# Kernel tuning notes

Hardware: AMD Instinct MI355X
Metric: run time of the kernel (lower is better)

## Reference

```python
import jax, jax.numpy as jnp
import numpy as np

B, T, H, D = 512, 256, 256, 3  # batch, seq_len, RNN_hid_dim, var_dim


def setup_inputs() -> dict:
    key = jax.random.key(0)
    ks = jax.random.split(key, 14)
    s = 1.0 / np.sqrt(H)  # PyTorch GRU init scale
    return {
        "X_p": jax.random.normal(ks[0], (B, T, D), jnp.float32),
        "X_f": jax.random.normal(ks[1], (B, T, D), jnp.float32),
        "noise": jax.random.normal(ks[2], (1, B, H), jnp.float32),
        # encoder GRU params (PyTorch layout: gates ordered r, z, n)
        "W_ih_enc": jax.random.uniform(ks[3], (3 * H, D), jnp.float32, -s, s),
        "W_hh_enc": jax.random.uniform(ks[4], (3 * H, H), jnp.float32, -s, s),
        "b_ih_enc": jax.random.uniform(ks[5], (3 * H,), jnp.float32, -s, s),
        "b_hh_enc": jax.random.uniform(ks[6], (3 * H,), jnp.float32, -s, s),
        # decoder GRU params
        "W_ih_dec": jax.random.uniform(ks[7], (3 * H, D), jnp.float32, -s, s),
        "W_hh_dec": jax.random.uniform(ks[8], (3 * H, H), jnp.float32, -s, s),
        "b_ih_dec": jax.random.uniform(ks[9], (3 * H,), jnp.float32, -s, s),
        "b_hh_dec": jax.random.uniform(ks[10], (3 * H,), jnp.float32, -s, s),
        # output projection
        "W_fc": jax.random.uniform(ks[11], (D, H), jnp.float32, -s, s),
        "b_fc": jax.random.uniform(ks[12], (D,), jnp.float32, -s, s),
    }


def _gru(x, h0, W_ih, W_hh, b_ih, b_hh):
    # x: [B, T, D]; h0: [B, H]. PyTorch GRU cell math, gate order r, z, n.
    xg = jnp.einsum('btd,gd->btg', x, W_ih) + b_ih  # [B, T, 3H] (one big GEMM)

    def step(h, xg_t):
        gh = h @ W_hh.T + b_hh                      # [B, 3H]
        xr, xz, xn = jnp.split(xg_t, 3, axis=-1)
        hr, hz, hn = jnp.split(gh, 3, axis=-1)
        r = jax.nn.sigmoid(xr + hr)
        z = jax.nn.sigmoid(xz + hz)
        n = jnp.tanh(xn + r * hn)
        h_new = (1.0 - z) * n + z * h
        return h_new, h_new

    hT, ys = jax.lax.scan(step, h0, jnp.swapaxes(xg, 0, 1))  # scan over T
    return jnp.swapaxes(ys, 0, 1), hT  # [B, T, H], [B, H]


def reference(X_p, X_f, noise, W_ih_enc, W_hh_enc, b_ih_enc, b_hh_enc,
              W_ih_dec, W_hh_dec, b_ih_dec, b_hh_dec, W_fc, b_fc):
    h0 = jnp.zeros((X_p.shape[0], W_hh_enc.shape[1]), X_p.dtype)
    _, h_t = _gru(X_p, h0, W_ih_enc, W_hh_enc, b_ih_enc, b_hh_enc)
    hidden = h_t + noise[0]                                   # h_t: [B,H], noise: [1,B,H]
    # shift right by one timestep, zero-fill first step
    X_f_shft = jnp.concatenate(
        [jnp.zeros_like(X_f[:, :1, :]), X_f[:, :-1, :]], axis=1)
    Y_f, _ = _gru(X_f_shft, hidden, W_ih_dec, W_hh_dec, b_ih_dec, b_hh_dec)
    return jnp.einsum('bth,dh->btd', Y_f, W_fc) + b_fc        # [B, T, D]
```

## Files before the change

### kernel.cpp

```cpp
#include <hip/hip_runtime.h>


#define B_TOT 512
#define T_LEN 256
#define HID 256
#define NBATCH 16
#define NB 4
#define NTHREADS 1024
#define NBLK (B_TOT / NB)

#define WR_OFF 0
#define H_OFF  32768
#define X_OFF  40960
#define RD_OFF 57408
#define SMEM_SHORTS (RD_OFF + 16 * 512)
#define SMEM_BYTES  (SMEM_SHORTS * 2)

#define XT 64
#define XSLOTS (T_LEN + 1)
#define HBUF (NBATCH * HID)

typedef __attribute__((ext_vector_type(4))) float f32x4;
typedef __attribute__((ext_vector_type(8))) short shortx8;
typedef __attribute__((ext_vector_type(4))) short i16x4;
typedef __attribute__((ext_vector_type(4))) unsigned short ushortx4;
typedef __attribute__((ext_vector_type(8))) unsigned short ushortx8;

#if __has_builtin(__builtin_amdgcn_mfma_f32_16x16x16_bf16)
#define HAVE_K16 1
#define MFMA_X(A, B, C) __builtin_amdgcn_mfma_f32_16x16x16_bf16((A), (B), (C), 0, 0, 0)
#elif __has_builtin(__builtin_amdgcn_mfma_f32_16x16x16bf16_1k)
#define HAVE_K16 1
#define MFMA_X(A, B, C) __builtin_amdgcn_mfma_f32_16x16x16bf16_1k((A), (B), (C), 0, 0, 0)
#else
#define HAVE_K16 0
#endif

__device__ __forceinline__ unsigned short f2bf(float x) {
    unsigned u = __float_as_uint(x);
    u += 0x7FFF + ((u >> 16) & 1);
    return (unsigned short)(u >> 16);
}
__device__ __forceinline__ float bf2f(unsigned short s) {
    return __uint_as_float(((unsigned)s) << 16);
}
__device__ __forceinline__ float fastrcp(float x) {
#if __has_builtin(__builtin_amdgcn_rcpf)
    return __builtin_amdgcn_rcpf(x);
#else
    return 1.0f / x;
#endif
}
__device__ __forceinline__ float exp2raw(float y) {
#if __has_builtin(__builtin_amdgcn_exp2f)
    return __builtin_amdgcn_exp2f(y);
#else
    return __expf(y * 0.69314718056f);
#endif
}
__device__ __forceinline__ float sigmoid_(float x) {
    return fastrcp(1.0f + exp2raw(x * -1.44269504f));
}
__device__ __forceinline__ float tanh_(float x) {
    return 2.0f * fastrcp(1.0f + exp2raw(x * -2.88539008f)) - 1.0f;
}

__global__ __launch_bounds__(256) void prep_wr(
    const float* __restrict__ Whh_enc, const float* __restrict__ Whh_dec,
    unsigned short* __restrict__ wr_enc, unsigned short* __restrict__ wr_dec)
{
    int idx = blockIdx.x * 256 + threadIdx.x;
    int gru = idx >> 12;
    int rem = idx & 4095;
    int lane = rem & 63;
    int kk = (rem >> 6) & 3;
    int ht = rem >> 8;
    const float* W = gru ? Whh_dec : Whh_enc;
    unsigned short* dst = gru ? wr_dec : wr_enc;
    int row = ht * 16 + (lane & 15);
    int col = (kk + 4) * 32 + (lane >> 4) * 8;
    const float* src = W + (size_t)row * 256 + col;
    ushortx8 v;
    #pragma unroll
    for (int j = 0; j < 8; ++j) v[j] = f2bf(src[j]);
    *(ushortx8*)(dst + (size_t)rem * 8) = v;
}

template<int IS_DEC>
__global__ __launch_bounds__(NTHREADS, 4) void gru_persistent(
    const float* __restrict__ X,
    const float* __restrict__ W_hh,
    const float* __restrict__ W_ih,
    const float* __restrict__ b_ih,
    const float* __restrict__ b_hh,
    const unsigned short* __restrict__ Wr4,
    const float* __restrict__ h_in,
    const float* __restrict__ noise,
    float* __restrict__ h_out,
    unsigned short* __restrict__ Yout)
{
    extern __shared__ unsigned short smem[];
    unsigned short* shWr = smem + WR_OFF;
    unsigned short* shH  = smem + H_OFF;
    unsigned short* shX  = smem + X_OFF;
    unsigned short* shRd = smem + RD_OFF;

    const int tid  = threadIdx.x;
    const int g    = blockIdx.x;
    const int w    = tid >> 6;
    const int lane = tid & 63;
    const int c    = lane & 15;
    const int q    = lane >> 4;
    const int ht   = w;
    const int cv   = lane >> 4;
    const int din  = lane & 15;
    const int d_glob = ht * 16 + din;

    for (int idx = tid; idx < NBATCH * XSLOTS; idx += NTHREADS) {
        int t = idx >> 4, cc = idx & 15;
        int ts = IS_DEC ? (t - 1) : t;
        float x0 = 0.0f, x1 = 0.0f, x2 = 0.0f;
        if (cc < NB && ts >= 0 && ts < T_LEN) {
            const float* xp = X + ((size_t)(g * NB + cc) * T_LEN + ts) * 3;
            x0 = xp[0]; x1 = xp[1]; x2 = xp[2];
        }
        ushortx4 v = {f2bf(x0), f2bf(x1), f2bf(x2), (unsigned short)0x3F80};
        *(ushortx4*)&shX[t * XT + cc * 4] = v;
    }

    {
        int row = ht * 16 + c;
        const float* wp = W_hh + (size_t)row * 256 + q * 8;
        #pragma unroll
        for (int k = 0; k < 4; ++k) {
            const f32x4* p = (const f32x4*)(wp + k * 32);
            f32x4 f0 = p[0];
            f32x4 f1 = p[1];
            shortx8 a;
            a[0] = (short)f2bf(f0[0]); a[1] = (short)f2bf(f0[1]);
            a[2] = (short)f2bf(f0[2]); a[3] = (short)f2bf(f0[3]);
            a[4] = (short)f2bf(f1[0]); a[5] = (short)f2bf(f1[1]);
            a[6] = (short)f2bf(f1[2]); a[7] = (short)f2bf(f1[3]);
            *(shortx8*)&shWr[((ht * 4 + k) * 64 + lane) * 8] = a;
        }
    }

    shortx8 Wf[2][8];
    #pragma unroll
    for (int gg = 0; gg < 2; ++gg) {
        int row = (gg + 1) * 256 + ht * 16 + c;
        const float* wp = W_hh + (size_t)row * 256 + q * 8;
        #pragma unroll
        for (int k = 0; k < 8; ++k) {
            const f32x4* p = (const f32x4*)(wp + k * 32);
            f32x4 f0 = p[0];
            f32x4 f1 = p[1];
            shortx8 a;
            a[0] = (short)f2bf(f0[0]); a[1] = (short)f2bf(f0[1]);
            a[2] = (short)f2bf(f0[2]); a[3] = (short)f2bf(f0[3]);
            a[4] = (short)f2bf(f1[0]); a[5] = (short)f2bf(f1[1]);
            a[6] = (short)f2bf(f1[2]); a[7] = (short)f2bf(f1[3]);
            Wf[gg][k] = a;
        }
    }

#if HAVE_K16
    i16x4 ax[3];
#else
    shortx8 ax[3];
#endif
    {
        int rr_ = ht * 16 + c;
        int rowr = rr_, rowz = 256 + rr_, rown = 512 + rr_;
        short r0 = 0, r1 = 0, r2 = 0, r3 = 0, z0 = 0, z1 = 0, z2 = 0, z3 = 0;
        short n0 = 0, n1 = 0, n2 = 0, n3 = 0;
        if (q == 0) {
            r0 = (short)f2bf(W_ih[rowr * 3 + 0]);
            r1 = (short)f2bf(W_ih[rowr * 3 + 1]);
            r2 = (short)f2bf(W_ih[rowr * 3 + 2]);
            r3 = (short)f2bf(b_ih[rowr] + b_hh[rowr]);
            z0 = (short)f2bf(W_ih[rowz * 3 + 0]);
            z1 = (short)f2bf(W_ih[rowz * 3 + 1]);
            z2 = (short)f2bf(W_ih[rowz * 3 + 2]);
            z3 = (short)f2bf(b_ih[rowz] + b_hh[rowz]);
            n0 = (short)f2bf(W_ih[rown * 3 + 0]);
            n1 = (short)f2bf(W_ih[rown * 3 + 1]);
            n2 = (short)f2bf(W_ih[rown * 3 + 2]);
            n3 = (short)f2bf(b_ih[rown]);
        }
#if HAVE_K16
        ax[0] = i16x4{r0, r1, r2, r3};
        ax[1] = i16x4{z0, z1, z2, z3};
        ax[2] = i16x4{n0, n1, n2, n3};
#else
        ax[0] = shortx8{r0, r1, r2, r3, 0, 0, 0, 0};
        ax[1] = shortx8{z0, z1, z2, z3, 0, 0, 0, 0};
        ax[2] = shortx8{n0, n1, n2, n3, 0, 0, 0, 0};
#endif
    }

    f32x4 nhb = *(const f32x4*)(b_hh + 512 + ht * 16 + q * 4);

    const int offv = ht * 256 + (din >> 3) * 128 + ((din >> 2) & 1) * 4
                   + cv * 8 + (din & 3);

    {
        const ushortx8 z8 = {0, 0, 0, 0, 0, 0, 0, 0};
        *(ushortx8*)&shH[tid * 8] = z8;
    }
    __syncthreads();

    float hold = 0.0f;
    if (IS_DEC) {
        int b = g * NB + cv;
        hold = h_in[(size_t)b * HID + d_glob] + noise[(size_t)b * HID + d_glob];
        shH[offv] = f2bf(hold);
    }

    unsigned short* yp = nullptr;
    if (IS_DEC)
        yp = Yout + ((size_t)g * T_LEN * NB + cv) * HID + d_glob;

    __syncthreads();

    const f32x4 zc = {0.0f, 0.0f, 0.0f, 0.0f};

    f32x4 acc0, acc1, acc2, acc3;
    {
#if HAVE_K16
        i16x4 bx = *(const i16x4*)&shX[c * 4];
        acc0 = MFMA_X(ax[0], bx, zc);
        acc1 = MFMA_X(ax[1], bx, zc);
        acc3 = MFMA_X(ax[2], bx, zc);
#else
        ushortx4 xv = *(const ushortx4*)&shX[c * 4];
        shortx8 bx = (q == 0)
            ? shortx8{(short)xv[0], (short)xv[1], (short)xv[2], (short)xv[3], 0, 0, 0, 0}
            : shortx8{0, 0, 0, 0, 0, 0, 0, 0};
        acc0 = __builtin_amdgcn_mfma_f32_16x16x32_bf16(ax[0], bx, zc, 0, 0, 0);
        acc1 = __builtin_amdgcn_mfma_f32_16x16x32_bf16(ax[1], bx, zc, 0, 0, 0);
        acc3 = __builtin_amdgcn_mfma_f32_16x16x32_bf16(ax[2], bx, zc, 0, 0, 0);
#endif
    }

    const int bbase = q * 128 + c * 8;
    const unsigned short* ab = shWr + ((size_t)(ht * 4) * 64 + lane) * 8;
    const unsigned short* gb = Wr4 + ((size_t)(ht * 4) * 64 + lane) * 8;
    unsigned short* shRd_w = shRd + w * 512;

    int xidx = XT + c * 4;

    for (int t = 0; t < T_LEN; ++t) {
        const unsigned short* brow = shH + (t & 1) * HBUF + bbase;
        unsigned short* hn = shH + ((t + 1) & 1) * HBUF;

        shortx8 gr[4];
        #pragma unroll
        for (int kk = 0; kk < 4; ++kk)
            gr[kk] = *(const shortx8*)(gb + kk * 512);

        acc2 = nhb;

        #pragma unroll
        for (int k = 0; k < 4; ++k) {
            shortx8 bf = *(const shortx8*)(brow + k * 512);
            shortx8 ar = *(const shortx8*)(ab + k * 512);
            acc0 = __builtin_amdgcn_mfma_f32_16x16x32_bf16(ar,       bf, acc0, 0, 0, 0);
            acc1 = __builtin_amdgcn_mfma_f32_16x16x32_bf16(Wf[0][k], bf, acc1, 0, 0, 0);
            acc2 = __builtin_amdgcn_mfma_f32_16x16x32_bf16(Wf[1][k], bf, acc2, 0, 0, 0);
        }
        #pragma unroll
        for (int k = 4; k < 8; ++k) {
            shortx8 bf = *(const shortx8*)(brow + k * 512);
            acc0 = __builtin_amdgcn_mfma_f32_16x16x32_bf16(gr[k - 4], bf, acc0, 0, 0, 0);
            acc1 = __builtin_amdgcn_mfma_f32_16x16x32_bf16(Wf[0][k],  bf, acc1, 0, 0, 0);
            acc2 = __builtin_amdgcn_mfma_f32_16x16x32_bf16(Wf[1][k],  bf, acc2, 0, 0, 0);
        }

        if (c < NB) {
            #pragma unroll
            for (int r = 0; r < 4; ++r) {
                f32x4 v = {acc0[r], acc1[r], acc2[r], acc3[r]};
                *(f32x4*)&shRd_w[(c * 16 + q * 4 + r) * 8] = v;
            }
        }

#if HAVE_K16
        i16x4 bxn = *(const i16x4*)&shX[xidx];
#else
        ushortx4 xvn = *(const ushortx4*)&shX[xidx];
        shortx8 bxn = (q == 0)
            ? shortx8{(short)xvn[0], (short)xvn[1], (short)xvn[2], (short)xvn[3], 0, 0, 0, 0}
            : shortx8{0, 0, 0, 0, 0, 0, 0, 0};
#endif
        xidx += XT;

#if HAVE_K16
        acc0 = MFMA_X(ax[0], bxn, zc);
        acc1 = MFMA_X(ax[1], bxn, zc);
        acc3 = MFMA_X(ax[2], bxn, zc);
#else
        acc0 = __builtin_amdgcn_mfma_f32_16x16x32_bf16(ax[0], bxn, zc, 0, 0, 0);
        acc1 = __builtin_amdgcn_mfma_f32_16x16x32_bf16(ax[1], bxn, zc, 0, 0, 0);
        acc3 = __builtin_amdgcn_mfma_f32_16x16x32_bf16(ax[2], bxn, zc, 0, 0, 0);
#endif

        {
            f32x4 av = *(const f32x4*)&shRd_w[lane * 8];
            float rr = sigmoid_(av[0]);
            float zz = sigmoid_(av[1]);
            float nn = tanh_(av[3] + rr * av[2]);
            float ho = nn + zz * (hold - nn);
            hold = ho;
            unsigned short hb = f2bf(ho);
            hn[offv] = hb;
            if (IS_DEC) {
                *yp = hb;
                yp += NB * HID;
            }
        }
        __syncthreads();
    }

    if (!IS_DEC) {
        h_out[(size_t)(g * NB + cv) * HID + d_glob] = hold;
    }
}

__global__ __launch_bounds__(256) void proj_kernel(
    const unsigned short* __restrict__ Y, const float* __restrict__ W_fc,
    const float* __restrict__ b_fc, float* __restrict__ out)
{
    int row = blockIdx.x * 256 + threadIdx.x;
    int b4 = row & (NB - 1);
    int gt = row >> 2;
    int t = gt & (T_LEN - 1);
    int g = gt >> 8;
    const unsigned short* y = Y + (size_t)row * HID;
    float a0 = b_fc[0], a1 = b_fc[1], a2 = b_fc[2];
    #pragma unroll 4
    for (int k8 = 0; k8 < 32; ++k8) {
        ushortx8 v = *(const ushortx8*)(y + k8 * 8);
        #pragma unroll
        for (int j = 0; j < 8; ++j) {
            float f = bf2f(v[j]);
            int k = k8 * 8 + j;
            a0 += f * W_fc[k];
            a1 += f * W_fc[256 + k];
            a2 += f * W_fc[512 + k];
        }
    }
    int batch = g * NB + b4;
    float* o = out + ((size_t)batch * T_LEN + t) * 3;
    o[0] = a0; o[1] = a1; o[2] = a2;
}

extern "C" void kernel_launch(void* const* d_in, const int* in_sizes, int n_in,
                              void* d_out, int out_size, void* d_ws, size_t ws_size,
                              hipStream_t stream)
{
    const float* X_p      = (const float*)d_in[0];
    const float* X_f      = (const float*)d_in[1];
    const float* noise    = (const float*)d_in[2];
    const float* W_ih_enc = (const float*)d_in[3];
    const float* W_hh_enc = (const float*)d_in[4];
    const float* b_ih_enc = (const float*)d_in[5];
    const float* b_hh_enc = (const float*)d_in[6];
    const float* W_ih_dec = (const float*)d_in[7];
    const float* W_hh_dec = (const float*)d_in[8];
    const float* b_ih_dec = (const float*)d_in[9];
    const float* b_hh_dec = (const float*)d_in[10];
    const float* W_fc     = (const float*)d_in[11];
    const float* b_fc     = (const float*)d_in[12];

    (void)hipFuncSetAttribute((const void*)&gru_persistent<0>,
                              hipFuncAttributeMaxDynamicSharedMemorySize, SMEM_BYTES);
    (void)hipFuncSetAttribute((const void*)&gru_persistent<1>,
                              hipFuncAttributeMaxDynamicSharedMemorySize, SMEM_BYTES);

    float* h_enc = (float*)d_ws;
    unsigned short* wr_enc = (unsigned short*)((char*)d_ws + (512u << 10));
    unsigned short* wr_dec = (unsigned short*)((char*)d_ws + (576u << 10));
    unsigned short* Yws    = (unsigned short*)((char*)d_ws + (640u << 10));

    hipLaunchKernelGGL(prep_wr, dim3(32), dim3(256), 0, stream,
        W_hh_enc, W_hh_dec, wr_enc, wr_dec);

    hipLaunchKernelGGL((gru_persistent<0>), dim3(NBLK), dim3(NTHREADS), SMEM_BYTES, stream,
        X_p, W_hh_enc, W_ih_enc, b_ih_enc, b_hh_enc, wr_enc,
        (const float*)nullptr, (const float*)nullptr, h_enc,
        (unsigned short*)nullptr);

    hipLaunchKernelGGL((gru_persistent<1>), dim3(NBLK), dim3(NTHREADS), SMEM_BYTES, stream,
        X_f, W_hh_dec, W_ih_dec, b_ih_dec, b_hh_dec, wr_dec,
        h_enc, noise, (float*)nullptr, Yws);

    hipLaunchKernelGGL(proj_kernel, dim3((B_TOT * T_LEN) / 256), dim3(256), 0, stream,
        Yws, W_fc, b_fc, (float*)d_out);
}
```

Measured before the change: 943.7 us.

## Keep all recurrent weights in registers and shrink LDS to the real batch

Moves the r-gate slice of W_hh, previously split between LDS and a global prep buffer, into registers, so each wave keeps all three gates' weight fragments resident. This drops the prep_wr kernel and the per-step global and LDS weight reads. The hidden-state and input buffers are sized for the 4 real batch columns instead of 16, so LDS use falls and the dynamic shared-memory attribute call is removed. It also adds an XOR swizzle on the gate-exchange scratch to avoid bank conflicts. The cost is higher register pressure from 24 resident weight fragments per thread, which may cause spills at 1024 threads.

```diff
diff --git a/kernel.cpp b/kernel.cpp
--- a/kernel.cpp
+++ b/kernel.cpp
@@ -9,16 +9,15 @@
 #define NTHREADS 1024
 #define NBLK (B_TOT / NB)
 
-#define WR_OFF 0
-#define H_OFF  32768
-#define X_OFF  40960
-#define RD_OFF 57408
+#define XSLOTS (T_LEN + 1)
+#define XT 16
+#define HBUF (NB * HID)
+
+#define H_OFF 0
+#define X_OFF (2 * HBUF)
+#define RD_OFF (X_OFF + XSLOTS * XT)
 #define SMEM_SHORTS (RD_OFF + 16 * 512)
 #define SMEM_BYTES  (SMEM_SHORTS * 2)
-
-#define XT 64
-#define XSLOTS (T_LEN + 1)
-#define HBUF (NBATCH * HID)
 
 typedef __attribute__((ext_vector_type(4))) float f32x4;
 typedef __attribute__((ext_vector_type(8))) short shortx8;
@@ -63,27 +62,6 @@
 }
 __device__ __forceinline__ float tanh_(float x) {
     return 2.0f * fastrcp(1.0f + exp2raw(x * -2.88539008f)) - 1.0f;
-}
-
-__global__ __launch_bounds__(256) void prep_wr(
-    const float* __restrict__ Whh_enc, const float* __restrict__ Whh_dec,
-    unsigned short* __restrict__ wr_enc, unsigned short* __restrict__ wr_dec)
-{
-    int idx = blockIdx.x * 256 + threadIdx.x;
-    int gru = idx >> 12;
-    int rem = idx & 4095;
-    int lane = rem & 63;
-    int kk = (rem >> 6) & 3;
-    int ht = rem >> 8;
-    const float* W = gru ? Whh_dec : Whh_enc;
-    unsigned short* dst = gru ? wr_dec : wr_enc;
-    int row = ht * 16 + (lane & 15);
-    int col = (kk + 4) * 32 + (lane >> 4) * 8;
-    const float* src = W + (size_t)row * 256 + col;
-    ushortx8 v;
-    #pragma unroll
-    for (int j = 0; j < 8; ++j) v[j] = f2bf(src[j]);
-    *(ushortx8*)(dst + (size_t)rem * 8) = v;
 }
 
 template<int IS_DEC>
@@ -93,14 +71,12 @@
     const float* __restrict__ W_ih,
     const float* __restrict__ b_ih,
     const float* __restrict__ b_hh,
-    const unsigned short* __restrict__ Wr4,
     const float* __restrict__ h_in,
     const float* __restrict__ noise,
     float* __restrict__ h_out,
     unsigned short* __restrict__ Yout)
 {
     extern __shared__ unsigned short smem[];
-    unsigned short* shWr = smem + WR_OFF;
     unsigned short* shH  = smem + H_OFF;
     unsigned short* shX  = smem + X_OFF;
     unsigned short* shRd = smem + RD_OFF;
@@ -116,11 +92,11 @@
     const int din  = lane & 15;
     const int d_glob = ht * 16 + din;
 
-    for (int idx = tid; idx < NBATCH * XSLOTS; idx += NTHREADS) {
-        int t = idx >> 4, cc = idx & 15;
+    for (int idx = tid; idx < NB * XSLOTS; idx += NTHREADS) {
+        int t = idx >> 2, cc = idx & 3;
         int ts = IS_DEC ? (t - 1) : t;
         float x0 = 0.0f, x1 = 0.0f, x2 = 0.0f;
-        if (cc < NB && ts >= 0 && ts < T_LEN) {
+        if (ts >= 0 && ts < T_LEN) {
             const float* xp = X + ((size_t)(g * NB + cc) * T_LEN + ts) * 3;
             x0 = xp[0]; x1 = xp[1]; x2 = xp[2];
         }
@@ -128,27 +104,10 @@
         *(ushortx4*)&shX[t * XT + cc * 4] = v;
     }
 
-    {
-        int row = ht * 16 + c;
-        const float* wp = W_hh + (size_t)row * 256 + q * 8;
-        #pragma unroll
-        for (int k = 0; k < 4; ++k) {
-            const f32x4* p = (const f32x4*)(wp + k * 32);
-            f32x4 f0 = p[0];
-            f32x4 f1 = p[1];
-            shortx8 a;
-            a[0] = (short)f2bf(f0[0]); a[1] = (short)f2bf(f0[1]);
-            a[2] = (short)f2bf(f0[2]); a[3] = (short)f2bf(f0[3]);
-            a[4] = (short)f2bf(f1[0]); a[5] = (short)f2bf(f1[1]);
-            a[6] = (short)f2bf(f1[2]); a[7] = (short)f2bf(f1[3]);
-            *(shortx8*)&shWr[((ht * 4 + k) * 64 + lane) * 8] = a;
-        }
-    }
-
-    shortx8 Wf[2][8];
+    shortx8 Wf[3][8];
     #pragma unroll
-    for (int gg = 0; gg < 2; ++gg) {
-        int row = (gg + 1) * 256 + ht * 16 + c;
+    for (int gg = 0; gg < 3; ++gg) {
+        int row = gg * 256 + ht * 16 + c;
         const float* wp = W_hh + (size_t)row * 256 + q * 8;
         #pragma unroll
         for (int k = 0; k < 8; ++k) {
@@ -201,21 +160,14 @@
 
     f32x4 nhb = *(const f32x4*)(b_hh + 512 + ht * 16 + q * 4);
 
-    const int offv = ht * 256 + (din >> 3) * 128 + ((din >> 2) & 1) * 4
-                   + cv * 8 + (din & 3);
-
-    {
-        const ushortx8 z8 = {0, 0, 0, 0, 0, 0, 0, 0};
-        *(ushortx8*)&shH[tid * 8] = z8;
-    }
-    __syncthreads();
+    const int offv = (d_glob >> 3) * 32 + cv * 8 + (d_glob & 7);
 
     float hold = 0.0f;
     if (IS_DEC) {
         int b = g * NB + cv;
         hold = h_in[(size_t)b * HID + d_glob] + noise[(size_t)b * HID + d_glob];
-        shH[offv] = f2bf(hold);
-    }
+    }
+    shH[offv] = f2bf(hold);
 
     unsigned short* yp = nullptr;
     if (IS_DEC)
@@ -224,29 +176,32 @@
     __syncthreads();
 
     const f32x4 zc = {0.0f, 0.0f, 0.0f, 0.0f};
+    const shortx8 z8 = {0, 0, 0, 0, 0, 0, 0, 0};
 
     f32x4 acc0, acc1, acc2, acc3;
     {
 #if HAVE_K16
-        i16x4 bx = *(const i16x4*)&shX[c * 4];
+        i16x4 bx = {0, 0, 0, 0};
+        if (c < NB) bx = *(const i16x4*)&shX[c * 4];
         acc0 = MFMA_X(ax[0], bx, zc);
         acc1 = MFMA_X(ax[1], bx, zc);
         acc3 = MFMA_X(ax[2], bx, zc);
 #else
-        ushortx4 xv = *(const ushortx4*)&shX[c * 4];
-        shortx8 bx = (q == 0)
-            ? shortx8{(short)xv[0], (short)xv[1], (short)xv[2], (short)xv[3], 0, 0, 0, 0}
-            : shortx8{0, 0, 0, 0, 0, 0, 0, 0};
+        shortx8 bx = z8;
+        if (q == 0 && c < NB) {
+            ushortx4 xv = *(const ushortx4*)&shX[c * 4];
+            bx = shortx8{(short)xv[0], (short)xv[1], (short)xv[2], (short)xv[3],
+                         0, 0, 0, 0};
+        }
         acc0 = __builtin_amdgcn_mfma_f32_16x16x32_bf16(ax[0], bx, zc, 0, 0, 0);
         acc1 = __builtin_amdgcn_mfma_f32_16x16x32_bf16(ax[1], bx, zc, 0, 0, 0);
         acc3 = __builtin_amdgcn_mfma_f32_16x16x32_bf16(ax[2], bx, zc, 0, 0, 0);
 #endif
     }
 
-    const int bbase = q * 128 + c * 8;
-    const unsigned short* ab = shWr + ((size_t)(ht * 4) * 64 + lane) * 8;
-    const unsigned short* gb = Wr4 + ((size_t)(ht * 4) * 64 + lane) * 8;
+    const int bbase = q * 32 + c * 8;
     unsigned short* shRd_w = shRd + w * 512;
+    const int rdoff = ((lane ^ (lane >> 4)) << 3);
 
     int xidx = XT + c * 4;
 
@@ -254,44 +209,36 @@
         const unsigned short* brow = shH + (t & 1) * HBUF + bbase;
         unsigned short* hn = shH + ((t + 1) & 1) * HBUF;
 
-        shortx8 gr[4];
+        acc2 = nhb;
+
         #pragma unroll
-        for (int kk = 0; kk < 4; ++kk)
-            gr[kk] = *(const shortx8*)(gb + kk * 512);
-
-        acc2 = nhb;
-
-        #pragma unroll
-        for (int k = 0; k < 4; ++k) {
-            shortx8 bf = *(const shortx8*)(brow + k * 512);
-            shortx8 ar = *(const shortx8*)(ab + k * 512);
-            acc0 = __builtin_amdgcn_mfma_f32_16x16x32_bf16(ar,       bf, acc0, 0, 0, 0);
-            acc1 = __builtin_amdgcn_mfma_f32_16x16x32_bf16(Wf[0][k], bf, acc1, 0, 0, 0);
-            acc2 = __builtin_amdgcn_mfma_f32_16x16x32_bf16(Wf[1][k], bf, acc2, 0, 0, 0);
-        }
-        #pragma unroll
-        for (int k = 4; k < 8; ++k) {
-            shortx8 bf = *(const shortx8*)(brow + k * 512);
-            acc0 = __builtin_amdgcn_mfma_f32_16x16x32_bf16(gr[k - 4], bf, acc0, 0, 0, 0);
-            acc1 = __builtin_amdgcn_mfma_f32_16x16x32_bf16(Wf[0][k],  bf, acc1, 0, 0, 0);
-            acc2 = __builtin_amdgcn_mfma_f32_16x16x32_bf16(Wf[1][k],  bf, acc2, 0, 0, 0);
+        for (int k = 0; k < 8; ++k) {
+            shortx8 bf = z8;
+            if (c < NB) bf = *(const shortx8*)(brow + k * 128);
+            acc0 = __builtin_amdgcn_mfma_f32_16x16x32_bf16(Wf[0][k], bf, acc0, 0, 0, 0);
+            acc1 = __builtin_amdgcn_mfma_f32_16x16x32_bf16(Wf[1][k], bf, acc1, 0, 0, 0);
+            acc2 = __builtin_amdgcn_mfma_f32_16x16x32_bf16(Wf[2][k], bf, acc2, 0, 0, 0);
         }
 
         if (c < NB) {
             #pragma unroll
             for (int r = 0; r < 4; ++r) {
                 f32x4 v = {acc0[r], acc1[r], acc2[r], acc3[r]};
-                *(f32x4*)&shRd_w[(c * 16 + q * 4 + r) * 8] = v;
+                int e = c * 16 + q * 4 + r;
+                *(f32x4*)&shRd_w[(e ^ c) << 3] = v;
             }
         }
 
 #if HAVE_K16
-        i16x4 bxn = *(const i16x4*)&shX[xidx];
-#else
-        ushortx4 xvn = *(const ushortx4*)&shX[xidx];
-        shortx8 bxn = (q == 0)
-            ? shortx8{(short)xvn[0], (short)xvn[1], (short)xvn[2], (short)xvn[3], 0, 0, 0, 0}
-            : shortx8{0, 0, 0, 0, 0, 0, 0, 0};
+        i16x4 bxn = {0, 0, 0, 0};
+        if (c < NB) bxn = *(const i16x4*)&shX[xidx];
+#else
+        shortx8 bxn = z8;
+        if (q == 0 && c < NB) {
+            ushortx4 xvn = *(const ushortx4*)&shX[xidx];
+            bxn = shortx8{(short)xvn[0], (short)xvn[1], (short)xvn[2], (short)xvn[3],
+                          0, 0, 0, 0};
+        }
 #endif
         xidx += XT;
 
@@ -306,7 +253,7 @@
 #endif
 
         {
-            f32x4 av = *(const f32x4*)&shRd_w[lane * 8];
+            f32x4 av = *(const f32x4*)&shRd_w[rdoff];
             float rr = sigmoid_(av[0]);
             float zz = sigmoid_(av[1]);
             float nn = tanh_(av[3] + rr * av[2]);
@@ -373,26 +320,16 @@
     const float* W_fc     = (const float*)d_in[11];
     const float* b_fc     = (const float*)d_in[12];
 
-    (void)hipFuncSetAttribute((const void*)&gru_persistent<0>,
-                              hipFuncAttributeMaxDynamicSharedMemorySize, SMEM_BYTES);
-    (void)hipFuncSetAttribute((const void*)&gru_persistent<1>,
-                              hipFuncAttributeMaxDynamicSharedMemorySize, SMEM_BYTES);
-
     float* h_enc = (float*)d_ws;
-    unsigned short* wr_enc = (unsigned short*)((char*)d_ws + (512u << 10));
-    unsigned short* wr_dec = (unsigned short*)((char*)d_ws + (576u << 10));
-    unsigned short* Yws    = (unsigned short*)((char*)d_ws + (640u << 10));
-
-    hipLaunchKernelGGL(prep_wr, dim3(32), dim3(256), 0, stream,
-        W_hh_enc, W_hh_dec, wr_enc, wr_dec);
+    unsigned short* Yws = (unsigned short*)((char*)d_ws + (512u << 10));
 
     hipLaunchKernelGGL((gru_persistent<0>), dim3(NBLK), dim3(NTHREADS), SMEM_BYTES, stream,
-        X_p, W_hh_enc, W_ih_enc, b_ih_enc, b_hh_enc, wr_enc,
+        X_p, W_hh_enc, W_ih_enc, b_ih_enc, b_hh_enc,
         (const float*)nullptr, (const float*)nullptr, h_enc,
         (unsigned short*)nullptr);
 
     hipLaunchKernelGGL((gru_persistent<1>), dim3(NBLK), dim3(NTHREADS), SMEM_BYTES, stream,
-        X_f, W_hh_dec, W_ih_dec, b_ih_dec, b_hh_dec, wr_dec,
+        X_f, W_hh_dec, W_ih_dec, b_ih_dec, b_hh_dec,
         h_enc, noise, (float*)nullptr, Yws);
 
     hipLaunchKernelGGL(proj_kernel, dim3((B_TOT * T_LEN) / 256), dim3(256), 0, stream,
```

After: 1.457 ms. 1.54x slower.

## Compact GRU hidden/x smem to real batch, compute n-gate input in FP32 scalars

Applied to the files above, without the earlier changes.

Shrinks the shared-memory hidden-state and input buffers from a 16-column padded batch to the 4 real batch columns. Padded lanes now feed zeros to the MFMAs instead of loading from LDS. The n-gate input projection moves from an extra MFMA per step to a per-thread FP32 dot product with its bias, which drops one accumulator and keeps that term in higher precision. Also XOR-swizzles the reduction scratch writes and reads to avoid LDS bank conflicts, and relaxes launch bounds to one block per SM. The smaller LDS footprint and lower register pressure trade against extra branches on the B-operand loads.

```diff
diff --git a/kernel.cpp b/kernel.cpp
--- a/kernel.cpp
+++ b/kernel.cpp
@@ -9,16 +9,16 @@
 #define NTHREADS 1024
 #define NBLK (B_TOT / NB)
 
+#define XSLOTS (T_LEN + 1)
+#define XT 16
+#define HBUF (NB * HID)
+
 #define WR_OFF 0
 #define H_OFF  32768
-#define X_OFF  40960
-#define RD_OFF 57408
-#define SMEM_SHORTS (RD_OFF + 16 * 512)
+#define X_OFF  34816
+#define RD_OFF 38928
+#define SMEM_SHORTS 47120
 #define SMEM_BYTES  (SMEM_SHORTS * 2)
-
-#define XT 64
-#define XSLOTS (T_LEN + 1)
-#define HBUF (NBATCH * HID)
 
 typedef __attribute__((ext_vector_type(4))) float f32x4;
 typedef __attribute__((ext_vector_type(8))) short shortx8;
@@ -87,7 +87,7 @@
 }
 
 template<int IS_DEC>
-__global__ __launch_bounds__(NTHREADS, 4) void gru_persistent(
+__global__ __launch_bounds__(NTHREADS, 1) void gru_persistent(
     const float* __restrict__ X,
     const float* __restrict__ W_hh,
     const float* __restrict__ W_ih,
@@ -112,15 +112,15 @@
     const int c    = lane & 15;
     const int q    = lane >> 4;
     const int ht   = w;
-    const int cv   = lane >> 4;
-    const int din  = lane & 15;
+    const int cv   = q;
+    const int din  = c;
     const int d_glob = ht * 16 + din;
 
-    for (int idx = tid; idx < NBATCH * XSLOTS; idx += NTHREADS) {
-        int t = idx >> 4, cc = idx & 15;
+    for (int idx = tid; idx < NB * XSLOTS; idx += NTHREADS) {
+        int t = idx >> 2, cc = idx & 3;
         int ts = IS_DEC ? (t - 1) : t;
         float x0 = 0.0f, x1 = 0.0f, x2 = 0.0f;
-        if (cc < NB && ts >= 0 && ts < T_LEN) {
+        if (ts >= 0 && ts < T_LEN) {
             const float* xp = X + ((size_t)(g * NB + cc) * T_LEN + ts) * 3;
             x0 = xp[0]; x1 = xp[1]; x2 = xp[2];
         }
@@ -165,15 +165,14 @@
     }
 
 #if HAVE_K16
-    i16x4 ax[3];
-#else
-    shortx8 ax[3];
+    i16x4 ax[2];
+#else
+    shortx8 ax[2];
 #endif
     {
         int rr_ = ht * 16 + c;
-        int rowr = rr_, rowz = 256 + rr_, rown = 512 + rr_;
+        int rowr = rr_, rowz = 256 + rr_;
         short r0 = 0, r1 = 0, r2 = 0, r3 = 0, z0 = 0, z1 = 0, z2 = 0, z3 = 0;
-        short n0 = 0, n1 = 0, n2 = 0, n3 = 0;
         if (q == 0) {
             r0 = (short)f2bf(W_ih[rowr * 3 + 0]);
             r1 = (short)f2bf(W_ih[rowr * 3 + 1]);
@@ -183,39 +182,29 @@
             z1 = (short)f2bf(W_ih[rowz * 3 + 1]);
             z2 = (short)f2bf(W_ih[rowz * 3 + 2]);
             z3 = (short)f2bf(b_ih[rowz] + b_hh[rowz]);
-            n0 = (short)f2bf(W_ih[rown * 3 + 0]);
-            n1 = (short)f2bf(W_ih[rown * 3 + 1]);
-            n2 = (short)f2bf(W_ih[rown * 3 + 2]);
-            n3 = (short)f2bf(b_ih[rown]);
         }
 #if HAVE_K16
         ax[0] = i16x4{r0, r1, r2, r3};
         ax[1] = i16x4{z0, z1, z2, z3};
-        ax[2] = i16x4{n0, n1, n2, n3};
 #else
         ax[0] = shortx8{r0, r1, r2, r3, 0, 0, 0, 0};
         ax[1] = shortx8{z0, z1, z2, z3, 0, 0, 0, 0};
-        ax[2] = shortx8{n0, n1, n2, n3, 0, 0, 0, 0};
-#endif
-    }
-
-    f32x4 nhb = *(const f32x4*)(b_hh + 512 + ht * 16 + q * 4);
-
-    const int offv = ht * 256 + (din >> 3) * 128 + ((din >> 2) & 1) * 4
-                   + cv * 8 + (din & 3);
-
-    {
-        const ushortx8 z8 = {0, 0, 0, 0, 0, 0, 0, 0};
-        *(ushortx8*)&shH[tid * 8] = z8;
-    }
-    __syncthreads();
+#endif
+    }
+
+    float Wn0 = W_ih[(512 + d_glob) * 3 + 0];
+    float Wn1 = W_ih[(512 + d_glob) * 3 + 1];
+    float Wn2 = W_ih[(512 + d_glob) * 3 + 2];
+    float bihn = b_ih[512 + d_glob];
+    float bhn  = b_hh[512 + d_glob];
+    const int offv = (d_glob >> 3) * 32 + cv * 8 + (d_glob & 7);
 
     float hold = 0.0f;
     if (IS_DEC) {
-        int b = g * NB + cv;
-        hold = h_in[(size_t)b * HID + d_glob] + noise[(size_t)b * HID + d_glob];
-        shH[offv] = f2bf(hold);
-    }
+        size_t gi = (size_t)(g * NB + cv) * HID + d_glob;
+        hold = h_in[gi] + noise[gi];
+    }
+    shH[offv] = f2bf(hold);
 
     unsigned short* yp = nullptr;
     if (IS_DEC)
@@ -224,31 +213,35 @@
     __syncthreads();
 
     const f32x4 zc = {0.0f, 0.0f, 0.0f, 0.0f};
-
-    f32x4 acc0, acc1, acc2, acc3;
+    const shortx8 z8 = {0, 0, 0, 0, 0, 0, 0, 0};
+
+    f32x4 acc0, acc1, acc2;
     {
 #if HAVE_K16
-        i16x4 bx = *(const i16x4*)&shX[c * 4];
+        i16x4 bx = {0, 0, 0, 0};
+        if (c < NB) bx = *(const i16x4*)&shX[c * 4];
         acc0 = MFMA_X(ax[0], bx, zc);
         acc1 = MFMA_X(ax[1], bx, zc);
-        acc3 = MFMA_X(ax[2], bx, zc);
-#else
-        ushortx4 xv = *(const ushortx4*)&shX[c * 4];
-        shortx8 bx = (q == 0)
-            ? shortx8{(short)xv[0], (short)xv[1], (short)xv[2], (short)xv[3], 0, 0, 0, 0}
-            : shortx8{0, 0, 0, 0, 0, 0, 0, 0};
+#else
+        shortx8 bx = z8;
+        if (q == 0 && c < NB) {
+            ushortx4 xv = *(const ushortx4*)&shX[c * 4];
+            bx = shortx8{(short)xv[0], (short)xv[1], (short)xv[2], (short)xv[3],
+                         0, 0, 0, 0};
+        }
         acc0 = __builtin_amdgcn_mfma_f32_16x16x32_bf16(ax[0], bx, zc, 0, 0, 0);
         acc1 = __builtin_amdgcn_mfma_f32_16x16x32_bf16(ax[1], bx, zc, 0, 0, 0);
-        acc3 = __builtin_amdgcn_mfma_f32_16x16x32_bf16(ax[2], bx, zc, 0, 0, 0);
-#endif
-    }
-
-    const int bbase = q * 128 + c * 8;
+#endif
+    }
+
+    const int bbase = q * 32 + c * 8;
     const unsigned short* ab = shWr + ((size_t)(ht * 4) * 64 + lane) * 8;
     const unsigned short* gb = Wr4 + ((size_t)(ht * 4) * 64 + lane) * 8;
     unsigned short* shRd_w = shRd + w * 512;
+    const int rdoff = (((cv * 16 + din) ^ cv) << 3);
 
     int xidx = XT + c * 4;
+    int xvidx = cv * 4;
 
     for (int t = 0; t < T_LEN; ++t) {
         const unsigned short* brow = shH + (t & 1) * HBUF + bbase;
@@ -259,11 +252,12 @@
         for (int kk = 0; kk < 4; ++kk)
             gr[kk] = *(const shortx8*)(gb + kk * 512);
 
-        acc2 = nhb;
+        acc2 = zc;
 
         #pragma unroll
         for (int k = 0; k < 4; ++k) {
-            shortx8 bf = *(const shortx8*)(brow + k * 512);
+            shortx8 bf = z8;
+            if (c < NB) bf = *(const shortx8*)(brow + k * 128);
             shortx8 ar = *(const shortx8*)(ab + k * 512);
             acc0 = __builtin_amdgcn_mfma_f32_16x16x32_bf16(ar,       bf, acc0, 0, 0, 0);
             acc1 = __builtin_amdgcn_mfma_f32_16x16x32_bf16(Wf[0][k], bf, acc1, 0, 0, 0);
@@ -271,7 +265,8 @@
         }
         #pragma unroll
         for (int k = 4; k < 8; ++k) {
-            shortx8 bf = *(const shortx8*)(brow + k * 512);
+            shortx8 bf = z8;
+            if (c < NB) bf = *(const shortx8*)(brow + k * 128);
             acc0 = __builtin_amdgcn_mfma_f32_16x16x32_bf16(gr[k - 4], bf, acc0, 0, 0, 0);
             acc1 = __builtin_amdgcn_mfma_f32_16x16x32_bf16(Wf[0][k],  bf, acc1, 0, 0, 0);
             acc2 = __builtin_amdgcn_mfma_f32_16x16x32_bf16(Wf[1][k],  bf, acc2, 0, 0, 0);
@@ -280,36 +275,43 @@
         if (c < NB) {
             #pragma unroll
             for (int r = 0; r < 4; ++r) {
-                f32x4 v = {acc0[r], acc1[r], acc2[r], acc3[r]};
-                *(f32x4*)&shRd_w[(c * 16 + q * 4 + r) * 8] = v;
+                f32x4 v = {acc0[r], acc1[r], acc2[r], 0.0f};
+                int e = c * 16 + q * 4 + r;
+                *(f32x4*)&shRd_w[(e ^ c) << 3] = v;
             }
         }
 
+        ushortx4 xval = *(const ushortx4*)&shX[xvidx];
+        xvidx += XT;
+
 #if HAVE_K16
-        i16x4 bxn = *(const i16x4*)&shX[xidx];
-#else
-        ushortx4 xvn = *(const ushortx4*)&shX[xidx];
-        shortx8 bxn = (q == 0)
-            ? shortx8{(short)xvn[0], (short)xvn[1], (short)xvn[2], (short)xvn[3], 0, 0, 0, 0}
-            : shortx8{0, 0, 0, 0, 0, 0, 0, 0};
+        i16x4 bxn = {0, 0, 0, 0};
+        if (c < NB) bxn = *(const i16x4*)&shX[xidx];
+#else
+        shortx8 bxn = z8;
+        if (q == 0 && c < NB) {
+            ushortx4 xvn = *(const ushortx4*)&shX[xidx];
+            bxn = shortx8{(short)xvn[0], (short)xvn[1], (short)xvn[2], (short)xvn[3],
+                          0, 0, 0, 0};
+        }
 #endif
         xidx += XT;
 
 #if HAVE_K16
         acc0 = MFMA_X(ax[0], bxn, zc);
         acc1 = MFMA_X(ax[1], bxn, zc);
-        acc3 = MFMA_X(ax[2], bxn, zc);
 #else
         acc0 = __builtin_amdgcn_mfma_f32_16x16x32_bf16(ax[0], bxn, zc, 0, 0, 0);
         acc1 = __builtin_amdgcn_mfma_f32_16x16x32_bf16(ax[1], bxn, zc, 0, 0, 0);
-        acc3 = __builtin_amdgcn_mfma_f32_16x16x32_bf16(ax[2], bxn, zc, 0, 0, 0);
 #endif
 
         {
-            f32x4 av = *(const f32x4*)&shRd_w[lane * 8];
+            f32x4 av = *(const f32x4*)&shRd_w[rdoff];
+            float x0 = bf2f(xval[0]), x1 = bf2f(xval[1]), x2 = bf2f(xval[2]);
+            float nx = Wn0 * x0 + Wn1 * x1 + Wn2 * x2 + bihn;
             float rr = sigmoid_(av[0]);
             float zz = sigmoid_(av[1]);
-            float nn = tanh_(av[3] + rr * av[2]);
+            float nn = tanh_(nx + rr * (av[2] + bhn));
             float ho = nn + zz * (hold - nn);
             hold = ho;
             unsigned short hb = f2bf(ho);
```

Result: faster. 877.6 us (-7.0%).
